# Kernel optimization log

Measured on AMD Instinct MI355X. Metric: run time of the kernel, lower is better.

## Reference

```python
import jax, jax.numpy as jnp
import numpy as np

NUM_HEADS = 16


def setup_inputs() -> dict:
    rng = jax.random.key(0)
    ks = jax.random.split(rng, 11)
    T, B, E = 1024, 4, 1024
    s = E ** -0.5  # weight init scale
    return {
        "query": jax.random.normal(ks[0], (T, B, E), jnp.float32),
        "key": jax.random.normal(ks[1], (T, B, E), jnp.float32),
        "value": jax.random.normal(ks[2], (T, B, E), jnp.float32),
        "q_proj_weight": jax.random.normal(ks[3], (E, E), jnp.float32) * s,
        "k_proj_weight1": jax.random.normal(ks[4], (E, E), jnp.float32) * s,
        "k_proj_weight2": jax.random.normal(ks[5], (E, E), jnp.float32) * s,
        "v_proj_weight": jax.random.normal(ks[6], (E, E), jnp.float32) * s,
        "in_proj_bias": jax.random.normal(ks[7], (4 * E,), jnp.float32) * 0.02,
        "out_proj_weight": jax.random.normal(ks[8], (E, E), jnp.float32) * s,
        "out_proj_bias": jax.random.normal(ks[9], (E,), jnp.float32) * 0.02,
        "pi": jax.random.uniform(ks[10], (2, NUM_HEADS), jnp.float32, 0.3, 0.7),
    }


def reference(query, key, value, q_proj_weight, k_proj_weight1, k_proj_weight2,
              v_proj_weight, in_proj_bias, out_proj_weight, out_proj_bias, pi):
    T, Bz, E = query.shape
    H = NUM_HEADS
    hd = E // H
    scaling = hd ** -0.5

    b_q, b_k1, b_k2, b_v = jnp.split(in_proj_bias, 4)
    q = query @ q_proj_weight.T + b_q
    k1 = key @ k_proj_weight1.T + b_k1
    k2 = key @ k_proj_weight2.T + b_k2
    v = value @ v_proj_weight.T + b_v

    def heads(x):  # (S, B, E) -> (B*H, S, hd)
        S = x.shape[0]
        return x.reshape(S, Bz * H, hd).transpose(1, 0, 2)

    q, k1, k2, v = heads(q), heads(k1), heads(k2), heads(v)

    def sqdist(a, b):  # (B*H, Nt, hd), (B*H, Ns, hd) -> (B*H, Nt, Ns)
        a2 = jnp.sum(a * a, axis=-1)
        b2 = jnp.sum(b * b, axis=-1)
        ab = jnp.einsum('btd,bsd->bts', a, b)
        return a2[:, :, None] + b2[:, None, :] - 2.0 * ab

    e1 = jnp.exp(-scaling / 2.0 * sqdist(q, k1))
    e2 = jnp.exp(-3.0 * scaling / 2.0 * sqdist(q, k2))

    pi1 = jnp.clip(jnp.abs(pi[0]), 1e-6, 2.0)  # (H,)
    pi2 = jnp.clip(jnp.abs(pi[1]), 1e-6, 2.0)

    Nt, Ns = e1.shape[1], e1.shape[2]
    attn = (e1.reshape(Bz, H, Nt, Ns) * pi1[None, :, None, None]
            + e2.reshape(Bz, H, Nt, Ns) * pi2[None, :, None, None])
    attn = attn.reshape(Bz * H, Nt, Ns)
    attn = attn / (jnp.sum(attn, axis=-1, keepdims=True) + 1e-6)

    out = jnp.einsum('bts,bsd->btd', attn, v)        # (B*H, Nt, hd)
    out = out.transpose(1, 0, 2).reshape(T, Bz, E)   # (T, B, E)
    return out @ out_proj_weight.T + out_proj_bias
```

## Files before the change

kernel.cpp:

```cpp
#include <hip/hip_runtime.h>
#include <hip/hip_bf16.h>

#define T_DIM 1024
#define B_DIM 4
#define E_DIM 1024
#define H_DIM 16
#define HD    64
#define M_DIM (T_DIM * B_DIM)

typedef __hip_bfloat16 bf16;
typedef __bf16 bf16x8 __attribute__((ext_vector_type(8)));
typedef __bf16 bf16x4 __attribute__((ext_vector_type(4)));
typedef __bf16 bf16x2 __attribute__((ext_vector_type(2)));
typedef float  f32x4  __attribute__((ext_vector_type(4)));

#define P4S ((size_t)M_DIM * E_DIM)
#define P1S ((size_t)E_DIM * E_DIM)

__global__ __launch_bounds__(256) void cvt_all(
    const float* __restrict__ q, const float* __restrict__ k,
    const float* __restrict__ v, const float* __restrict__ w0,
    const float* __restrict__ w1, const float* __restrict__ w2,
    const float* __restrict__ w3, const float* __restrict__ w4,
    __bf16* __restrict__ dst)
{
  size_t i = ((size_t)blockIdx.x * 256 + threadIdx.x) * 8;
  const float* src;
  size_t off;
  if (i < P4S)            { src = q; off = i; }
  else if (i < 2 * P4S)   { src = k; off = i - P4S; }
  else if (i < 3 * P4S)   { src = v; off = i - 2 * P4S; }
  else {
    size_t j = i - 3 * P4S;
    int wsel = (int)(j >> 20);
    off = j & (P1S - 1);
    const float* ws[5] = {w0, w1, w2, w3, w4};
    src = ws[wsel];
  }
  float4 a = *(const float4*)(src + off);
  float4 b = *(const float4*)(src + off + 4);
  bf16x8 o;
  o[0] = (__bf16)a.x; o[1] = (__bf16)a.y; o[2] = (__bf16)a.z; o[3] = (__bf16)a.w;
  o[4] = (__bf16)b.x; o[5] = (__bf16)b.y; o[6] = (__bf16)b.z; o[7] = (__bf16)b.w;
  *(bf16x8*)(dst + i) = o;
}

__device__ __forceinline__ void load_lds16(const __bf16* g, __bf16* l) {
  __builtin_amdgcn_global_load_lds(
      (__attribute__((address_space(1))) void*)(void*)g,
      (__attribute__((address_space(3))) void*)l, 16, 0, 0);
}

__device__ __forceinline__ void stage_half(
    int H, const __bf16* __restrict__ X, const __bf16* __restrict__ W,
    int bm, int bn, __bf16* As, __bf16* Bs, int tid)
{
  if (H >= 64) return;
  const int T  = H >> 2;
  const int h  = H & 3;
  const int rh = (h & 1) * 128;
  const __bf16* src = (h < 2) ? X : W;
  const int rbase   = (h < 2) ? bm : bn;
  __bf16* lb = ((h < 2) ? As : Bs) + (T & 1) * 16384;
#pragma unroll
  for (int li = 0; li < 2; ++li) {
    int r  = rh + li * 64 + (tid >> 3);
    int gc = (tid & 7) ^ (r & 7);
    load_lds16(src + (size_t)(rbase + r) * E_DIM + T * 64 + gc * 8,
               lb + (rh + li * 64) * 64 + tid * 8);
  }
}

#define RD(base, row, c) \
  (*(const bf16x8*)((base) + (row) * 64 + ((((c) ^ ((row) & 7))) << 3)))

__global__ __launch_bounds__(512, 2) void proj_gemm4(
    const __bf16* __restrict__ xbase, const __bf16* __restrict__ wbase,
    const float* __restrict__ bin, __bf16* __restrict__ cbase,
    float* __restrict__ qn_g, float* __restrict__ knr_g)
{
  __shared__ __bf16 lds[65536];
  __bf16* As = lds;
  __bf16* Bs = lds + 32768;

  const int z = blockIdx.z;
  const __bf16* X = xbase + ((z == 0) ? 0 : (z == 3) ? 2 * P4S : P4S);
  const __bf16* W = wbase + (size_t)z * P1S;
  const float* bias = bin + z * E_DIM;
  __bf16* C = cbase + (size_t)z * P4S;

  const int bm = blockIdx.x * 256;
  const int bn = blockIdx.y * 256;

  const int tid  = threadIdx.x;
  const int lane = tid & 63;
  const int w    = tid >> 6;
  const int wm   = w >> 2;
  const int wn   = w & 3;
  const int mrow = lane & 15, quad = lane >> 4;

  f32x4 acc[8][4];
#pragma unroll
  for (int m = 0; m < 8; ++m)
#pragma unroll
    for (int n = 0; n < 4; ++n) acc[m][n] = (f32x4)0.0f;

#pragma unroll
  for (int H = 0; H < 5; ++H) stage_half(H, X, W, bm, bn, As, Bs, tid);
  asm volatile("s_waitcnt vmcnt(2)" ::: "memory");
  __builtin_amdgcn_s_barrier();

  bf16x8 af[4][2];
  bf16x8 bq[4][2];

#pragma unroll 2
  for (int t = 0; t < 16; ++t) {
    const __bf16* Ab = As + (t & 1) * 16384;
    const __bf16* Bb = Bs + (t & 1) * 16384;

#pragma unroll
    for (int n = 0; n < 2; ++n)
#pragma unroll
      for (int kk = 0; kk < 2; ++kk)
        bq[n][kk] = RD(Bb, wn * 64 + n * 16 + mrow, kk * 4 + quad);
#pragma unroll
    for (int m = 0; m < 4; ++m)
#pragma unroll
      for (int kk = 0; kk < 2; ++kk)
        af[m][kk] = RD(Ab, wm * 128 + m * 16 + mrow, kk * 4 + quad);
    stage_half(4 * t + 5, X, W, bm, bn, As, Bs, tid);
    __builtin_amdgcn_s_barrier();
    asm volatile("s_waitcnt lgkmcnt(0)" ::: "memory");
    __builtin_amdgcn_s_setprio(1);
#pragma unroll
    for (int kk = 0; kk < 2; ++kk)
#pragma unroll
      for (int n = 0; n < 2; ++n)
#pragma unroll
        for (int m = 0; m < 4; ++m)
          acc[m][n] = __builtin_amdgcn_mfma_f32_16x16x32_bf16(
              af[m][kk], bq[n][kk], acc[m][n], 0, 0, 0);
    __builtin_amdgcn_s_setprio(0);
    __builtin_amdgcn_s_barrier();

#pragma unroll
    for (int n = 2; n < 4; ++n)
#pragma unroll
      for (int kk = 0; kk < 2; ++kk)
        bq[n][kk] = RD(Bb, wn * 64 + n * 16 + mrow, kk * 4 + quad);
    stage_half(4 * t + 6, X, W, bm, bn, As, Bs, tid);
    __builtin_amdgcn_s_barrier();
    asm volatile("s_waitcnt lgkmcnt(0)" ::: "memory");
    __builtin_amdgcn_s_setprio(1);
#pragma unroll
    for (int kk = 0; kk < 2; ++kk)
#pragma unroll
      for (int n = 2; n < 4; ++n)
#pragma unroll
        for (int m = 0; m < 4; ++m)
          acc[m][n] = __builtin_amdgcn_mfma_f32_16x16x32_bf16(
              af[m][kk], bq[n][kk], acc[m][n], 0, 0, 0);
    __builtin_amdgcn_s_setprio(0);
    __builtin_amdgcn_s_barrier();

#pragma unroll
    for (int m = 0; m < 4; ++m)
#pragma unroll
      for (int kk = 0; kk < 2; ++kk)
        af[m][kk] = RD(Ab, wm * 128 + 64 + m * 16 + mrow, kk * 4 + quad);
    stage_half(4 * t + 7, X, W, bm, bn, As, Bs, tid);
    __builtin_amdgcn_s_barrier();
    asm volatile("s_waitcnt lgkmcnt(0)" ::: "memory");
    __builtin_amdgcn_s_setprio(1);
#pragma unroll
    for (int kk = 0; kk < 2; ++kk)
#pragma unroll
      for (int n = 0; n < 2; ++n)
#pragma unroll
        for (int m = 0; m < 4; ++m)
          acc[4 + m][n] = __builtin_amdgcn_mfma_f32_16x16x32_bf16(
              af[m][kk], bq[n][kk], acc[4 + m][n], 0, 0, 0);
    __builtin_amdgcn_s_setprio(0);
    __builtin_amdgcn_s_barrier();

    stage_half(4 * t + 8, X, W, bm, bn, As, Bs, tid);
    __builtin_amdgcn_s_barrier();
    __builtin_amdgcn_s_setprio(1);
#pragma unroll
    for (int kk = 0; kk < 2; ++kk)
#pragma unroll
      for (int n = 2; n < 4; ++n)
#pragma unroll
        for (int m = 0; m < 4; ++m)
          acc[4 + m][n] = __builtin_amdgcn_mfma_f32_16x16x32_bf16(
              af[m][kk], bq[n][kk], acc[4 + m][n], 0, 0, 0);
    __builtin_amdgcn_s_setprio(0);
    if (t < 14)       { asm volatile("s_waitcnt vmcnt(2)" ::: "memory"); }
    else if (t == 14) { asm volatile("s_waitcnt vmcnt(0)" ::: "memory"); }
    __builtin_amdgcn_s_barrier();
  }

  f32x4 ns[8];
#pragma unroll
  for (int m = 0; m < 8; ++m) ns[m] = (f32x4)0.0f;
#pragma unroll
  for (int n = 0; n < 4; ++n) {
    int col = bn + wn * 64 + n * 16 + mrow;
    float bc = bias[col];
#pragma unroll
    for (int m = 0; m < 8; ++m) {
      int rbase = bm + wm * 128 + m * 16 + quad * 4;
#pragma unroll
      for (int r = 0; r < 4; ++r) {
        __bf16 xb = (__bf16)(acc[m][n][r] + bc);
        C[(size_t)(rbase + r) * E_DIM + col] = xb;
        float xv = (float)xb;
        ns[m][r] = fmaf(xv, xv, ns[m][r]);
      }
    }
  }
  if (z < 3) {
#pragma unroll
    for (int m = 0; m < 8; ++m)
#pragma unroll
      for (int d = 1; d < 16; d <<= 1) {
        f32x4 o;
#pragma unroll
        for (int r = 0; r < 4; ++r) o[r] = __shfl_xor(ns[m][r], d, 64);
        ns[m] += o;
      }
    if (mrow == 0) {
      int hh = (bn >> 6) + wn;
#pragma unroll
      for (int m = 0; m < 8; ++m) {
        int t = (bm >> 2) + wm * 32 + m * 4 + quad;
#pragma unroll
        for (int r = 0; r < 4; ++r) {
          int bhh = r * 16 + hh;
          float v = ns[m][r];
          if (z == 0)
            qn_g[bhh * 1024 + t] = v;
          else
            knr_g[bhh * 2048 + (t >> 5) * 64 + ((z == 2) ? 32 : 0)
                  + (t & 15) * 2 + ((t >> 4) & 1)] = v;
        }
      }
    }
  }
}

template <typename TO>
__device__ __forceinline__ void gemm_body(
    const __bf16* __restrict__ X, const __bf16* __restrict__ W,
    const float* __restrict__ bias, TO* __restrict__ C,
    int bm, int bn, int Ndim, int Kdim, __bf16* As, __bf16* Bs)
{
  const int tid  = threadIdx.x;
  const int lane = tid & 63;
  const int wave = tid >> 6;
  const int wy = (wave >> 1) * 64;
  const int wx = (wave & 1) * 64;
  const int mrow = lane & 15, quad = lane >> 4;

  const int srow = tid >> 2;
  const int ke   = (tid & 3) * 8;
  const __bf16* gA0 = X + (size_t)(bm + srow)      * Kdim + ke;
  const __bf16* gA1 = X + (size_t)(bm + srow + 64) * Kdim + ke;
  const __bf16* gB0 = W + (size_t)(bn + srow)      * Kdim + ke;
  const __bf16* gB1 = W + (size_t)(bn + srow + 64) * Kdim + ke;
  __bf16* lA0 = As + tid * 8;
  __bf16* lA1 = As + (tid + 256) * 8;
  __bf16* lB0 = Bs + tid * 8;
  __bf16* lB1 = Bs + (tid + 256) * 8;

  f32x4 acc[4][4];
#pragma unroll
  for (int i = 0; i < 4; ++i)
#pragma unroll
    for (int j = 0; j < 4; ++j) acc[i][j] = (f32x4)0.0f;

  for (int k0 = 0; k0 < Kdim; k0 += 32) {
    __syncthreads();
    load_lds16(gA0 + k0, lA0);
    load_lds16(gA1 + k0, lA1);
    load_lds16(gB0 + k0, lB0);
    load_lds16(gB1 + k0, lB1);
    __syncthreads();
    bf16x8 af[4], bf[4];
#pragma unroll
    for (int i = 0; i < 4; ++i)
      af[i] = *(const bf16x8*)(As + (wy + i * 16 + mrow) * 32 + quad * 8);
#pragma unroll
    for (int j = 0; j < 4; ++j)
      bf[j] = *(const bf16x8*)(Bs + (wx + j * 16 + mrow) * 32 + quad * 8);
#pragma unroll
    for (int i = 0; i < 4; ++i)
#pragma unroll
      for (int j = 0; j < 4; ++j)
        acc[i][j] = __builtin_amdgcn_mfma_f32_16x16x32_bf16(af[i], bf[j], acc[i][j], 0, 0, 0);
  }

#pragma unroll
  for (int j = 0; j < 4; ++j) {
    int col = bn + wx + j * 16 + mrow;
    float bc = bias[col];
#pragma unroll
    for (int i = 0; i < 4; ++i) {
      int rbase = bm + wy + i * 16 + quad * 4;
#pragma unroll
      for (int r = 0; r < 4; ++r)
        C[(size_t)(rbase + r) * Ndim + col] = (TO)(acc[i][j][r] + bc);
    }
  }
}

__global__ __launch_bounds__(256) void out_gemm(
    const __bf16* __restrict__ X, const __bf16* __restrict__ W,
    const float* __restrict__ bias, float* __restrict__ C)
{
  __shared__ __bf16 As[128 * 32];
  __shared__ __bf16 Bs[128 * 32];
  gemm_body<float>(X, W, bias, C, blockIdx.x * 128, blockIdx.y * 128,
                   E_DIM, E_DIM, As, Bs);
}

__global__ __launch_bounds__(256) void vt_only(
    const __bf16* __restrict__ Vp, __bf16* __restrict__ Vt_g)
{
  __shared__ __bf16 tile[64][88];
  const int tid = threadIdx.x;
  const int bh = blockIdx.x & 63, kt = blockIdx.x >> 6;
  const int b = bh >> 4, h = bh & 15;
  {
    int s = tid >> 2, d0 = (tid & 3) * 16;
    const __bf16* src = Vp + (size_t)((kt * 64 + s) * 4 + b) * 1024 + h * 64 + d0;
    *(bf16x8*)(&tile[s][d0])     = *(const bf16x8*)(src);
    *(bf16x8*)(&tile[s][d0 + 8]) = *(const bf16x8*)(src + 8);
  }
  __syncthreads();
#pragma unroll
  for (int c = 0; c < 2; ++c) {
    int idx = tid * 2 + c;
    int d = idx >> 3, u0 = (idx & 7) * 8;
    bf16x8 o;
#pragma unroll
    for (int i = 0; i < 8; ++i) {
      int u = u0 + i;
      int s = (u >> 5) * 32 + ((u & 31) >> 1) + (u & 1) * 16;
      o[i] = tile[s][d];
    }
    *(bf16x8*)(Vt_g + ((size_t)bh * 64 + d) * 1024 + kt * 64 + u0) = o;
  }
}

__global__ __launch_bounds__(256, 2) void mgk_attn_mfma(
    const __bf16* __restrict__ Qp, const __bf16* __restrict__ K1p,
    const __bf16* __restrict__ K2p, const __bf16* __restrict__ Vt_g,
    const float* __restrict__ qn_g, const float* __restrict__ knr_g,
    const float* __restrict__ pi, __bf16* __restrict__ AO)
{
  __shared__ __bf16 lds[20480];
  __bf16* Pl  = lds + 12288;
  float*  knl = (float*)(lds + 16384);

  const int bid = blockIdx.x;
  const int bh  = (bid & 7) * 8 + ((bid >> 3) & 7);
  const int qt  = bid >> 6;
  const int b = bh >> 4, h = bh & 15;
  const int tid = threadIdx.x, lane = tid & 63, w = tid >> 6;
  const int mrow = lane & 15, quad = lane >> 4;

  const float cl1 = 0.0625f * 1.4426950408889634f;
  const float cl2 = 0.1875f * 1.4426950408889634f;
  const float L1 = 2.0f * cl1, L2 = 2.0f * cl2;
  const float p1 = fminf(fmaxf(fabsf(pi[h]), 1e-6f), 2.0f);
  const float p2 = fminf(fmaxf(fabsf(pi[H_DIM + h]), 1e-6f), 2.0f);
  const float lp1 = __log2f(p1), lp2 = __log2f(p2);
  const int hoff = h * 64;

  bf16x8 af[2][2];
  f32x4 aq2[2];
#pragma unroll
  for (int m = 0; m < 2; ++m) {
    const __bf16* qp = Qp + (size_t)((qt * 128 + w * 32 + m * 16 + mrow) * 4 + b) * 1024
                       + hoff + quad * 8;
    af[m][0] = *(const bf16x8*)(qp);
    af[m][1] = *(const bf16x8*)(qp + 32);
    f32x4 qnv = *(const f32x4*)(qn_g + bh * 1024 + qt * 128 + w * 32 + m * 16 + quad * 4);
#pragma unroll
    for (int r = 0; r < 4; ++r) aq2[m][r] = fmaf(cl1 - cl2, qnv[r], lp2);
  }

  const int srow = tid >> 3;
  const int pch  = tid & 7;
  const int gcK  = pch ^ (srow & 7);
  const __bf16* gK1 = K1p + (size_t)(srow * 4 + b) * 1024 + hoff + gcK * 8;
  const __bf16* gK2 = K2p + (size_t)(srow * 4 + b) * 1024 + hoff + gcK * 8;
  const int vcl = pch ^ (srow & 7);
  const int vd  = (vcl >> 2) * 32 + srow;
  const int vu0 = (vcl & 3) * 8;
  const __bf16* gVt = Vt_g + ((size_t)bh * 64 + vd) * 1024 + vu0;

#define STAGE_T(kt_, bsel_) do {                                              \
    __bf16* bb_ = lds + (bsel_) * 6144;                                       \
    load_lds16(gK1 + (size_t)(kt_) * 131072, bb_ + tid * 8);                  \
    load_lds16(gK2 + (size_t)(kt_) * 131072, bb_ + 2048 + tid * 8);           \
    load_lds16(gVt + (kt_) * 32,             bb_ + 4096 + tid * 8);           \
  } while (0)

  load_lds16((const __bf16*)(knr_g + bh * 2048 + tid * 4),
             (__bf16*)knl + tid * 8);
  load_lds16((const __bf16*)(knr_g + bh * 2048 + 1024 + tid * 4),
             (__bf16*)knl + 2048 + tid * 8);
  STAGE_T(0, 0);
  STAGE_T(1, 1);
  asm volatile("s_waitcnt vmcnt(3)" ::: "memory");
  __builtin_amdgcn_s_barrier();

  f32x4 oacc[2][4];
#pragma unroll
  for (int m = 0; m < 2; ++m)
#pragma unroll
    for (int j = 0; j < 4; ++j) oacc[m][j] = (f32x4)0.0f;
  f32x4 rsl[2] = {(f32x4)0.0f, (f32x4)0.0f};

  for (int i = 0; i < 32; ++i) {
    const __bf16* buf = lds + (i & 1) * 6144;
    const __bf16* K1s = buf;
    const __bf16* K2s = buf + 2048;
    const __bf16* Vts = buf + 4096;

    float2 f1 = *(const float2*)(knl + i * 64 + mrow * 2);
    float2 f2 = *(const float2*)(knl + i * 64 + 32 + mrow * 2);
    float nb1[2], s2v[2];
    nb1[0] = fmaf(-cl1, f1.x, lp1); nb1[1] = fmaf(-cl1, f1.y, lp1);
    s2v[0] = -cl2 * f2.x;           s2v[1] = -cl2 * f2.y;

    f32x4 acc1[2][2], acc2[2][2];
#pragma unroll
    for (int m = 0; m < 2; ++m)
#pragma unroll
      for (int j = 0; j < 2; ++j) { acc1[m][j] = (f32x4)0.0f; acc2[m][j] = (f32x4)0.0f; }
    __builtin_amdgcn_s_setprio(1);
#pragma unroll
    for (int kk = 0; kk < 2; ++kk)
#pragma unroll
      for (int j = 0; j < 2; ++j) {
        int row = j * 16 + mrow;
        int off = row * 64 + (((kk * 4 + quad) ^ (row & 7)) << 3);
        bf16x8 b1f = *(const bf16x8*)(K1s + off);
        bf16x8 b2f = *(const bf16x8*)(K2s + off);
#pragma unroll
        for (int m = 0; m < 2; ++m) {
          acc1[m][j] = __builtin_amdgcn_mfma_f32_16x16x32_bf16(af[m][kk], b1f, acc1[m][j], 0, 0, 0);
          acc2[m][j] = __builtin_amdgcn_mfma_f32_16x16x32_bf16(af[m][kk], b2f, acc2[m][j], 0, 0, 0);
        }
      }
    __builtin_amdgcn_s_setprio(0);

#pragma unroll
    for (int m = 0; m < 2; ++m) {
      f32x4 pj[2];
#pragma unroll
      for (int j = 0; j < 2; ++j) {
        f32x4 p;
#pragma unroll
        for (int r = 0; r < 4; ++r) {
          float e1 = __builtin_amdgcn_exp2f(fmaf(L1, acc1[m][j][r], nb1[j]));
          float e2 = __builtin_amdgcn_exp2f(fmaf(L2, acc2[m][j][r], s2v[j] + aq2[m][r]));
          p[r] = e1 + e2;
        }
        pj[j] = p;
        rsl[m] += p;
      }
#pragma unroll
      for (int r = 0; r < 4; ++r) {
        int row  = quad * 4 + r;
        int phys = (m * 4 + (mrow >> 2)) ^ (row & 7);
        bf16x2 pk; pk[0] = (__bf16)pj[0][r]; pk[1] = (__bf16)pj[1][r];
        *(bf16x2*)(Pl + w * 1024 + row * 64 + phys * 8 + (mrow & 3) * 2) = pk;
      }
    }

    bf16x8 pf[2];
#pragma unroll
    for (int m = 0; m < 2; ++m)
      pf[m] = *(const bf16x8*)(Pl + w * 1024 + mrow * 64
                               + (((m * 4 + quad) ^ (mrow & 7)) << 3));
    __builtin_amdgcn_s_setprio(1);
#pragma unroll
    for (int j = 0; j < 4; ++j) {
      int rowv = (j & 1) * 16 + mrow;
      int cl   = (j >> 1) * 4 + quad;
      bf16x8 vf = *(const bf16x8*)(Vts + rowv * 64 + ((cl ^ (rowv & 7)) << 3));
#pragma unroll
      for (int m = 0; m < 2; ++m)
        oacc[m][j] = __builtin_amdgcn_mfma_f32_16x16x32_bf16(pf[m], vf, oacc[m][j], 0, 0, 0);
    }
    __builtin_amdgcn_s_setprio(0);

    if (i < 31) {
      asm volatile("s_waitcnt lgkmcnt(0)" ::: "memory");
      __builtin_amdgcn_s_barrier();
      if (i < 30) {
        STAGE_T(i + 2, i & 1);
        asm volatile("s_waitcnt vmcnt(3)" ::: "memory");
      } else {
        asm volatile("s_waitcnt vmcnt(0)" ::: "memory");
      }
      __builtin_amdgcn_s_barrier();
    }
  }
#undef STAGE_T

#pragma unroll
  for (int m = 0; m < 2; ++m) {
#pragma unroll
    for (int d = 1; d < 16; d <<= 1) {
      f32x4 o;
#pragma unroll
      for (int r = 0; r < 4; ++r) o[r] = __shfl_xor(rsl[m][r], d, 64);
      rsl[m] += o;
    }
    f32x4 inv;
#pragma unroll
    for (int r = 0; r < 4; ++r) inv[r] = 1.0f / (rsl[m][r] + 1e-6f);
#pragma unroll
    for (int j = 0; j < 4; ++j) {
      int col = hoff + j * 16 + mrow;
#pragma unroll
      for (int r = 0; r < 4; ++r) {
        int t = qt * 128 + w * 32 + m * 16 + quad * 4 + r;
        AO[(size_t)(t * 4 + b) * 1024 + col] = (__bf16)(oacc[m][j][r] * inv[r]);
      }
    }
  }
}

extern "C" void kernel_launch(void* const* d_in, const int* in_sizes, int n_in,
                              void* d_out, int out_size, void* d_ws, size_t ws_size,
                              hipStream_t stream) {
  const float* query = (const float*)d_in[0];
  const float* key   = (const float*)d_in[1];
  const float* value = (const float*)d_in[2];
  const float* Wq    = (const float*)d_in[3];
  const float* Wk1   = (const float*)d_in[4];
  const float* Wk2   = (const float*)d_in[5];
  const float* Wv    = (const float*)d_in[6];
  const float* bin   = (const float*)d_in[7];
  const float* Wo    = (const float*)d_in[8];
  const float* bo    = (const float*)d_in[9];
  const float* pi    = (const float*)d_in[10];
  float* out = (float*)d_out;

  __bf16* qc  = (__bf16*)d_ws;
  __bf16* wq  = qc  + 3 * P4S;
  __bf16* wo  = wq  + 4 * P1S;
  __bf16* Qp  = wq  + 5 * P1S;
  __bf16* K1p = Qp  + P4S;
  __bf16* K2p = K1p + P4S;
  __bf16* Vp  = K2p + P4S;
  __bf16* AO  = Vp  + P4S;
  float*  qn_g = (float*)(AO + P4S);
  float*  knr  = qn_g + 64 * 1024;
  __bf16* Vt_g = qc;

  cvt_all<<<8704, 256, 0, stream>>>(query, key, value, Wq, Wk1, Wk2, Wv, Wo, qc);

  proj_gemm4<<<dim3(M_DIM / 256, E_DIM / 256, 4), 512, 0, stream>>>(
      qc, wq, bin, Qp, qn_g, knr);

  vt_only<<<1024, 256, 0, stream>>>(Vp, Vt_g);

  mgk_attn_mfma<<<512, 256, 0, stream>>>(
      Qp, K1p, K2p, Vt_g, qn_g, knr, pi, AO);

  out_gemm<<<dim3(M_DIM / 128, E_DIM / 128), 256, 0, stream>>>(AO, wo, bo, out);
}
```

Before: 246.1 us.

## Move row-norm computation out of projection GEMM epilogue and use MFMA row sums

Removes the squared-norm reduction (shuffles and scattered stores) from the projection GEMM epilogue and computes the Q/K1/K2 per-head norms in a separate pass folded into the V-transpose kernel. The attention kernel now gets softmax-style row sums by multiplying the bf16 probability tile by a ones vector on the MFMA units instead of accumulating in VALU and reducing with shuffles at the end. This is meant to cut register pressure and epilogue work in the GEMM and VALU work in the attention inner loop, at the cost of re-reading the projected Q/K tensors from memory and summing the rounded bf16 probabilities rather than the fp32 ones.

```diff
diff --git a/kernel.cpp b/kernel.cpp
--- a/kernel.cpp
+++ b/kernel.cpp
@@ -76,8 +76,7 @@
 
 __global__ __launch_bounds__(512, 2) void proj_gemm4(
     const __bf16* __restrict__ xbase, const __bf16* __restrict__ wbase,
-    const float* __restrict__ bin, __bf16* __restrict__ cbase,
-    float* __restrict__ qn_g, float* __restrict__ knr_g)
+    const float* __restrict__ bin, __bf16* __restrict__ cbase)
 {
   __shared__ __bf16 lds[65536];
   __bf16* As = lds;
@@ -200,9 +199,6 @@
     __builtin_amdgcn_s_barrier();
   }
 
-  f32x4 ns[8];
-#pragma unroll
-  for (int m = 0; m < 8; ++m) ns[m] = (f32x4)0.0f;
 #pragma unroll
   for (int n = 0; n < 4; ++n) {
     int col = bn + wn * 64 + n * 16 + mrow;
@@ -211,40 +207,8 @@
     for (int m = 0; m < 8; ++m) {
       int rbase = bm + wm * 128 + m * 16 + quad * 4;
 #pragma unroll
-      for (int r = 0; r < 4; ++r) {
-        __bf16 xb = (__bf16)(acc[m][n][r] + bc);
-        C[(size_t)(rbase + r) * E_DIM + col] = xb;
-        float xv = (float)xb;
-        ns[m][r] = fmaf(xv, xv, ns[m][r]);
-      }
-    }
-  }
-  if (z < 3) {
-#pragma unroll
-    for (int m = 0; m < 8; ++m)
-#pragma unroll
-      for (int d = 1; d < 16; d <<= 1) {
-        f32x4 o;
-#pragma unroll
-        for (int r = 0; r < 4; ++r) o[r] = __shfl_xor(ns[m][r], d, 64);
-        ns[m] += o;
-      }
-    if (mrow == 0) {
-      int hh = (bn >> 6) + wn;
-#pragma unroll
-      for (int m = 0; m < 8; ++m) {
-        int t = (bm >> 2) + wm * 32 + m * 4 + quad;
-#pragma unroll
-        for (int r = 0; r < 4; ++r) {
-          int bhh = r * 16 + hh;
-          float v = ns[m][r];
-          if (z == 0)
-            qn_g[bhh * 1024 + t] = v;
-          else
-            knr_g[bhh * 2048 + (t >> 5) * 64 + ((z == 2) ? 32 : 0)
-                  + (t & 15) * 2 + ((t >> 4) & 1)] = v;
-        }
-      }
+      for (int r = 0; r < 4; ++r)
+        C[(size_t)(rbase + r) * E_DIM + col] = (__bf16)(acc[m][n][r] + bc);
     }
   }
 }
@@ -324,12 +288,38 @@
                    E_DIM, E_DIM, As, Bs);
 }
 
-__global__ __launch_bounds__(256) void vt_only(
-    const __bf16* __restrict__ Vp, __bf16* __restrict__ Vt_g)
+__global__ __launch_bounds__(256) void norms_vt(
+    const __bf16* __restrict__ Qp, const __bf16* __restrict__ K1p,
+    const __bf16* __restrict__ K2p, const __bf16* __restrict__ Vp,
+    float* __restrict__ qn, float* __restrict__ knr,
+    __bf16* __restrict__ Vt_g)
 {
   __shared__ __bf16 tile[64][88];
   const int tid = threadIdx.x;
-  const int bh = blockIdx.x & 63, kt = blockIdx.x >> 6;
+  if (blockIdx.x < 768) {
+    int id = blockIdx.x * 256 + tid;
+    int which = id >> 16;
+    int r = id & 65535;
+    int bh = r >> 10, t = r & 1023;
+    int b = bh >> 4, h = bh & 15;
+    const __bf16* src = (which == 0) ? Qp : ((which == 1) ? K1p : K2p);
+    const __bf16* p = src + (size_t)(t * 4 + b) * 1024 + h * 64;
+    float s = 0.f;
+#pragma unroll
+    for (int c = 0; c < 8; ++c) {
+      bf16x8 v = *(const bf16x8*)(p + c * 8);
+#pragma unroll
+      for (int j = 0; j < 8; ++j) { float x = (float)v[j]; s += x * x; }
+    }
+    if (which == 0)
+      qn[bh * 1024 + t] = s;
+    else
+      knr[bh * 2048 + (t >> 5) * 64 + ((which == 2) ? 32 : 0)
+          + (t & 15) * 2 + ((t >> 4) & 1)] = s;
+    return;
+  }
+  int bid = blockIdx.x - 768;
+  const int bh = bid & 63, kt = bid >> 6;
   const int b = bh >> 4, h = bh & 15;
   {
     int s = tid >> 2, d0 = (tid & 3) * 16;
@@ -390,6 +380,10 @@
 #pragma unroll
     for (int r = 0; r < 4; ++r) aq2[m][r] = fmaf(cl1 - cl2, qnv[r], lp2);
   }
+
+  bf16x8 onesv;
+#pragma unroll
+  for (int i = 0; i < 8; ++i) onesv[i] = (__bf16)1.0f;
 
   const int srow = tid >> 3;
   const int pch  = tid & 7;
@@ -422,7 +416,7 @@
   for (int m = 0; m < 2; ++m)
 #pragma unroll
     for (int j = 0; j < 4; ++j) oacc[m][j] = (f32x4)0.0f;
-  f32x4 rsl[2] = {(f32x4)0.0f, (f32x4)0.0f};
+  f32x4 osum[2] = {(f32x4)0.0f, (f32x4)0.0f};
 
   for (int i = 0; i < 32; ++i) {
     const __bf16* buf = lds + (i & 1) * 6144;
@@ -471,7 +465,6 @@
           p[r] = e1 + e2;
         }
         pj[j] = p;
-        rsl[m] += p;
       }
 #pragma unroll
       for (int r = 0; r < 4; ++r) {
@@ -488,6 +481,9 @@
       pf[m] = *(const bf16x8*)(Pl + w * 1024 + mrow * 64
                                + (((m * 4 + quad) ^ (mrow & 7)) << 3));
     __builtin_amdgcn_s_setprio(1);
+#pragma unroll
+    for (int m = 0; m < 2; ++m)
+      osum[m] = __builtin_amdgcn_mfma_f32_16x16x32_bf16(pf[m], onesv, osum[m], 0, 0, 0);
 #pragma unroll
     for (int j = 0; j < 4; ++j) {
       int rowv = (j & 1) * 16 + mrow;
@@ -515,16 +511,9 @@
 
 #pragma unroll
   for (int m = 0; m < 2; ++m) {
-#pragma unroll
-    for (int d = 1; d < 16; d <<= 1) {
-      f32x4 o;
-#pragma unroll
-      for (int r = 0; r < 4; ++r) o[r] = __shfl_xor(rsl[m][r], d, 64);
-      rsl[m] += o;
-    }
     f32x4 inv;
 #pragma unroll
-    for (int r = 0; r < 4; ++r) inv[r] = 1.0f / (rsl[m][r] + 1e-6f);
+    for (int r = 0; r < 4; ++r) inv[r] = 1.0f / (osum[m][r] + 1e-6f);
 #pragma unroll
     for (int j = 0; j < 4; ++j) {
       int col = hoff + j * 16 + mrow;
@@ -567,10 +556,10 @@
 
   cvt_all<<<8704, 256, 0, stream>>>(query, key, value, Wq, Wk1, Wk2, Wv, Wo, qc);
 
-  proj_gemm4<<<dim3(M_DIM / 256, E_DIM / 256, 4), 512, 0, stream>>>(
-      qc, wq, bin, Qp, qn_g, knr);
-
-  vt_only<<<1024, 256, 0, stream>>>(Vp, Vt_g);
+  proj_gemm4<<<dim3(M_DIM / 256, E_DIM / 256, 4), 512, 0, stream>>>(qc, wq, bin, Qp);
+
+  norms_vt<<<768 + 1024, 256, 0, stream>>>(Qp, K1p, K2p, Vp,
+                                           qn_g, knr, Vt_g);
 
   mgk_attn_mfma<<<512, 256, 0, stream>>>(
       Qp, K1p, K2p, Vt_g, qn_g, knr, pi, AO);
```

After: 238.8 us. -3.0%, faster.
